# Kernel optimization log

Hardware: AMD Instinct MI355X
Metric: run time of the kernel (lower is better)

## Reference

```python
import jax, jax.numpy as jnp
import numpy as np

EPS = 1e-7


def setup_inputs() -> dict:
    key = jax.random.key(0)
    kx, kw, kv, kp = jax.random.split(key, 4)
    B, H, Wd, d, V, O = 4, 64, 64, 64, 64, 64
    X = jax.random.normal(kx, (B, H, Wd, d), dtype=jnp.float32)
    W = jax.random.normal(kw, (d, V), dtype=jnp.float32)
    # positive variances (kmeans-style init in original); avoid near-zero divisors
    variance = jax.random.uniform(kv, (d, V), dtype=jnp.float32) + 0.5
    weight = jax.random.normal(kp, (d, O), dtype=jnp.float32) * (1.0 / np.sqrt(d))
    return {"X": X, "W": W, "variance": variance, "weight": weight}


def reference(X, W, variance, weight):
    B, H, Wd, d = X.shape
    V = W.shape[1]
    HW = H * Wd
    Xf = X.reshape(B, HW, d)
    # Faithful replication of torch code: extend = tile(X, V) over last axis,
    # then reshape (d*V) -> (d, V) with k = a*V + c, so the X component at
    # grid position (a, c) is X[..., (a*V + c) % d].
    idx = (jnp.arange(d)[:, None] * V + jnp.arange(V)[None, :]) % d  # (d, V)
    Xg = Xf[:, :, idx]                      # (B, HW, d, V)
    q1 = (Xg - W) / variance                # (B, HW, d, V), broadcast (d,V)
    q = jnp.sum(q1 * q1, axis=2)            # (B, HW, V) squared Mahalanobis-ish dist
    q = q - jnp.min(q, axis=-1, keepdims=True)
    Q = jnp.exp(-0.5 * q)
    Q = Q / jnp.sum(Q, axis=-1, keepdims=True)          # soft assignment (B, HW, V)
    # Raw row-major reinterpretation (B, HW, d*V) -> (B, d, HW, V), as in torch
    z = q1.reshape(B, d, HW, V)
    zQ = z * Q[:, None, :, :]                            # (B, d, HW, V)
    z = jnp.sum(zQ, axis=2)                              # (B, d, V)
    Qsum = jnp.sum(Q, axis=1)                            # (B, V)
    z = (z + EPS) / (Qsum[:, None, :] + EPS)
    norm = jnp.sum(z * z, axis=1, keepdims=True)         # (B, 1, V)
    Z = z / norm                                          # (B, d, V)
    Adj = jnp.einsum('bdv,bdu->bvu', Z, Z)               # (B, V, V)
    out = jnp.einsum('bdv,do->bvo', Z, weight)           # (B, V, O)
    out = jnp.einsum('bvu,buo->bvo', Adj, out)           # (B, V, O)
    Zo = jax.nn.relu(out)
    Xn = jnp.einsum('bnv,bvo->bno', Q, Zo)               # (B, HW, O)
    return Xn.reshape(B, H, Wd, -1).transpose(0, 3, 1, 2)  # (B, O, H, W)
```

## Files before the change

### kernel.cpp

```cpp
#include <hip/hip_runtime.h>

#define HW 4096
#define EPSF 1e-7f

#define WS_S1  0
#define WS_S2P 16384
#define WS_QSP 32768
#define WS_Z   49152
#define WS_ZO  65536
#define WS_Q   81920

__device__ __forceinline__ void xr4(float4& v) {
    v.x += __shfl_xor(v.x, 16); v.y += __shfl_xor(v.y, 16);
    v.z += __shfl_xor(v.z, 16); v.w += __shfl_xor(v.w, 16);
    v.x += __shfl_xor(v.x, 32); v.y += __shfl_xor(v.y, 32);
    v.z += __shfl_xor(v.z, 32); v.w += __shfl_xor(v.w, 32);
}

__global__ __launch_bounds__(512) void kA(const float* __restrict__ X,
                                          const float* __restrict__ Wm,
                                          const float* __restrict__ var,
                                          float* __restrict__ ws) {
    int b = blockIdx.x >> 6, l = blockIdx.x & 63;
    int t = threadIdx.x;
    int wv = t >> 6, j = t & 63;
    int lane16 = t & 15, r0 = t >> 4;

    __shared__ __align__(16) float invl[64][64];
    __shared__ __align__(16) float wivl[64][64];
    __shared__ __align__(16) float abcA[64];
    __shared__ __align__(16) float abcB[64];
    __shared__ __align__(16) float abcC[64];
    __shared__ float red[3][8][64];
    __shared__ float4 red4[3][8][16];

    {
        float a = 0.f, bq = 0.f, c = 0.f;
#pragma unroll
        for (int k = 0; k < 8; k++) {
            int i = wv * 8 + k;
            float v   = var[i * 64 + j];
            float wvv = Wm[i * 64 + j];
            float iv  = 1.0f / v;
            invl[i][j] = iv; wivl[i][j] = wvv * iv;
            float iv2 = iv * iv;
            a += iv2; bq += wvv * iv2; c += wvv * wvv * iv2;
        }
        red[0][wv][j] = a; red[1][wv][j] = bq; red[2][wv][j] = c;
    }
    __syncthreads();
    if (t < 64) {
        float t0 = 0.f, t1 = 0.f, t2 = 0.f;
#pragma unroll
        for (int w = 0; w < 8; w++) { t0 += red[0][w][j]; t1 += red[1][w][j]; t2 += red[2][w][j]; }
        abcA[j] = t0; abcB[j] = t1; abcC[j] = t2;
    }
    __syncthreads();

    float4 A4 = *(const float4*)&abcA[lane16 * 4];
    float4 B4 = *(const float4*)&abcB[lane16 * 4];
    float4 C4 = *(const float4*)&abcC[lane16 * 4];
    float4 s1 = {0,0,0,0}, s2 = {0,0,0,0}, qsm = {0,0,0,0};
#pragma unroll
    for (int half = 0; half < 2; half++) {
        int rr = r0 + half * 32;
        int n  = l * 64 + rr;
        float4 x = *(const float4*)&X[((size_t)(b * HW) + n) * 64 + lane16 * 4];
        float4 q;
        q.x = fmaf(fmaf(A4.x, x.x, -2.0f * B4.x), x.x, C4.x);
        q.y = fmaf(fmaf(A4.y, x.y, -2.0f * B4.y), x.y, C4.y);
        q.z = fmaf(fmaf(A4.z, x.z, -2.0f * B4.z), x.z, C4.z);
        q.w = fmaf(fmaf(A4.w, x.w, -2.0f * B4.w), x.w, C4.w);
        float m = fminf(fminf(q.x, q.y), fminf(q.z, q.w));
        m = fminf(m, __shfl_xor(m, 1)); m = fminf(m, __shfl_xor(m, 2));
        m = fminf(m, __shfl_xor(m, 4)); m = fminf(m, __shfl_xor(m, 8));
        float4 e;
        e.x = __expf(-0.5f * (q.x - m)); e.y = __expf(-0.5f * (q.y - m));
        e.z = __expf(-0.5f * (q.z - m)); e.w = __expf(-0.5f * (q.w - m));
        float s = e.x + e.y + e.z + e.w;
        s += __shfl_xor(s, 1); s += __shfl_xor(s, 2);
        s += __shfl_xor(s, 4); s += __shfl_xor(s, 8);
        float rs = 1.0f / s;
        float4 Q4; Q4.x = e.x * rs; Q4.y = e.y * rs; Q4.z = e.z * rs; Q4.w = e.w * rs;
        *(float4*)&ws[WS_Q + ((size_t)(b * HW) + n) * 64 + lane16 * 4] = Q4;
        float4 iv4 = *(const float4*)&invl[rr][lane16 * 4];
        float4 wv4 = *(const float4*)&wivl[rr][lane16 * 4];
        s1.x = fmaf(iv4.x, Q4.x, s1.x); s1.y = fmaf(iv4.y, Q4.y, s1.y);
        s1.z = fmaf(iv4.z, Q4.z, s1.z); s1.w = fmaf(iv4.w, Q4.w, s1.w);
        s2.x = fmaf(wv4.x, Q4.x, s2.x); s2.y = fmaf(wv4.y, Q4.y, s2.y);
        s2.z = fmaf(wv4.z, Q4.z, s2.z); s2.w = fmaf(wv4.w, Q4.w, s2.w);
        qsm.x += Q4.x; qsm.y += Q4.y; qsm.z += Q4.z; qsm.w += Q4.w;
    }
    xr4(s1); xr4(s2); xr4(qsm);
    if ((t & 63) < 16) {
        red4[0][wv][lane16] = s1; red4[1][wv][lane16] = s2; red4[2][wv][lane16] = qsm;
    }
    __syncthreads();
    if (t < 64) {
        int jg = j >> 2, cc = j & 3;
        float t0 = 0.f, t1 = 0.f, t2 = 0.f;
#pragma unroll
        for (int w = 0; w < 8; w++) {
            t0 += ((const float*)&red4[0][w][jg])[cc];
            t1 += ((const float*)&red4[1][w][jg])[cc];
            t2 += ((const float*)&red4[2][w][jg])[cc];
        }
        int idx = (b * 64 + l) * 64 + j;
        ws[WS_S1  + idx] = t0;
        ws[WS_S2P + idx] = t1;
        ws[WS_QSP + idx] = t2;
    }
}

__global__ __launch_bounds__(512) void kB(const float* __restrict__ X,
                                          float* __restrict__ ws) {
    int b = blockIdx.x >> 6, h = blockIdx.x & 63;
    int t = threadIdx.x;
    int wv = t >> 6, j = t & 63;
    int lane16 = t & 15, lg = t >> 4;
    __shared__ float4 red4[3][8][16];
    float4 acc = {0,0,0,0}, ps2 = {0,0,0,0}, pqs = {0,0,0,0};
#pragma unroll
    for (int half = 0; half < 2; half++) {
        int l = lg + half * 32;
        float4 x  = *(const float4*)&X[((size_t)(b * HW) + h * 64 + l) * 64 + lane16 * 4];
        int idx = (b * 64 + l) * 64 + lane16 * 4;
        float4 s1 = *(const float4*)&ws[WS_S1 + idx];
        float4 a2 = *(const float4*)&ws[WS_S2P + idx];
        float4 a3 = *(const float4*)&ws[WS_QSP + idx];
        acc.x = fmaf(x.x, s1.x, acc.x); acc.y = fmaf(x.y, s1.y, acc.y);
        acc.z = fmaf(x.z, s1.z, acc.z); acc.w = fmaf(x.w, s1.w, acc.w);
        ps2.x += a2.x; ps2.y += a2.y; ps2.z += a2.z; ps2.w += a2.w;
        pqs.x += a3.x; pqs.y += a3.y; pqs.z += a3.z; pqs.w += a3.w;
    }
    xr4(acc); xr4(ps2); xr4(pqs);
    if ((t & 63) < 16) {
        red4[0][wv][lane16] = acc; red4[1][wv][lane16] = ps2; red4[2][wv][lane16] = pqs;
    }
    __syncthreads();
    if (t < 64) {
        int jg = j >> 2, cc = j & 3;
        float a = 0.f, s2 = 0.f, q = 0.f;
#pragma unroll
        for (int w = 0; w < 8; w++) {
            a  += ((const float*)&red4[0][w][jg])[cc];
            s2 += ((const float*)&red4[1][w][jg])[cc];
            q  += ((const float*)&red4[2][w][jg])[cc];
        }
        ws[WS_Z + (b * 64 + h) * 64 + j] = (a - s2 + EPSF) / (q + EPSF);
    }
}

__global__ __launch_bounds__(512) void kCD(const float* __restrict__ weight,
                                           float* __restrict__ ws) {
    int b = blockIdx.x >> 6, v = blockIdx.x & 63;
    int w8 = threadIdx.x >> 6, j = threadIdx.x & 63;
    __shared__ float zl[64][65];
    __shared__ float wl[64][65];
    __shared__ float red[8][64];
    __shared__ float sN[64], sin2[64], ghat[64], yv[64];
#pragma unroll
    for (int k = 0; k < 2; k++) {
        int fidx = (k * 512 + threadIdx.x) * 4;
        int r = fidx >> 6, cc = fidx & 63;
        float4 zv = *(const float4*)&ws[WS_Z + b * 4096 + fidx];
        float4 wv = *(const float4*)&weight[fidx];
        zl[r][cc] = zv.x; zl[r][cc+1] = zv.y; zl[r][cc+2] = zv.z; zl[r][cc+3] = zv.w;
        wl[r][cc] = wv.x; wl[r][cc+1] = wv.y; wl[r][cc+2] = wv.z; wl[r][cc+3] = wv.w;
    }
    __syncthreads();
    {
        float na = 0.f;
#pragma unroll
        for (int k = 0; k < 8; k++) { float zz = zl[w8 * 8 + k][j]; na = fmaf(zz, zz, na); }
        red[w8][j] = na;
        __syncthreads();
        if (threadIdx.x < 64) {
            float s = 0.f;
#pragma unroll
            for (int tt = 0; tt < 8; tt++) s += red[tt][j];
            sN[j] = s; sin2[j] = 1.0f / (s * s);
        }
        __syncthreads();
    }
    {
        float g = 0.f;
#pragma unroll
        for (int k = 0; k < 8; k++) { int d = w8 * 8 + k; g = fmaf(zl[d][v], zl[d][j], g); }
        red[w8][j] = g;
        __syncthreads();
        if (threadIdx.x < 64) {
            float s = 0.f;
#pragma unroll
            for (int tt = 0; tt < 8; tt++) s += red[tt][j];
            ghat[j] = s * sin2[j];
        }
        __syncthreads();
    }
    {
        float y = 0.f;
#pragma unroll
        for (int k = 0; k < 8; k++) { int u = w8 * 8 + k; y = fmaf(ghat[u], zl[j][u], y); }
        red[w8][j] = y;
        __syncthreads();
        if (threadIdx.x < 64) {
            float s = 0.f;
#pragma unroll
            for (int tt = 0; tt < 8; tt++) s += red[tt][j];
            yv[j] = s;
        }
        __syncthreads();
    }
    {
        float a = 0.f;
#pragma unroll
        for (int k = 0; k < 8; k++) { int d = w8 * 8 + k; a = fmaf(yv[d], wl[d][j], a); }
        red[w8][j] = a;
        __syncthreads();
        if (threadIdx.x < 64) {
            float s = 0.f;
#pragma unroll
            for (int tt = 0; tt < 8; tt++) s += red[tt][j];
            float r = s / sN[v];
            r = r > 0.f ? r : 0.f;
            ws[WS_ZO + (b * 64 + v) * 64 + j] = r;
        }
    }
}

__global__ __launch_bounds__(512) void kF(const float* __restrict__ ws,
                                          float* __restrict__ out) {
    int b = blockIdx.x >> 6, tb = blockIdx.x & 63;
    int nbase = tb * 64;
    int w8 = threadIdx.x >> 6, lane = threadIdx.x & 63;
    int o8 = w8 * 8;
    __shared__ float qs[64][65];
    __shared__ __align__(16) float zo[64][68];
#pragma unroll
    for (int k = 0; k < 2; k++) {
        int fidx = (k * 512 + threadIdx.x) * 4;
        int r = fidx >> 6, cc = fidx & 63;
        float4 qv = *(const float4*)&ws[WS_Q + ((size_t)(b * HW) + nbase + r) * 64 + cc];
        qs[r][cc] = qv.x; qs[r][cc+1] = qv.y; qs[r][cc+2] = qv.z; qs[r][cc+3] = qv.w;
        float4 zv = *(const float4*)&ws[WS_ZO + b * 4096 + fidx];
        zo[r][cc] = zv.x; zo[r][cc+1] = zv.y; zo[r][cc+2] = zv.z; zo[r][cc+3] = zv.w;
    }
    __syncthreads();
    float acc[8];
#pragma unroll
    for (int k = 0; k < 8; k++) acc[k] = 0.f;
#pragma unroll
    for (int v = 0; v < 64; v++) {
        float qv = qs[lane][v];
        float4 z0 = *(const float4*)&zo[v][o8];
        float4 z1 = *(const float4*)&zo[v][o8 + 4];
        acc[0] = fmaf(qv, z0.x, acc[0]);
        acc[1] = fmaf(qv, z0.y, acc[1]);
        acc[2] = fmaf(qv, z0.z, acc[2]);
        acc[3] = fmaf(qv, z0.w, acc[3]);
        acc[4] = fmaf(qv, z1.x, acc[4]);
        acc[5] = fmaf(qv, z1.y, acc[5]);
        acc[6] = fmaf(qv, z1.z, acc[6]);
        acc[7] = fmaf(qv, z1.w, acc[7]);
    }
#pragma unroll
    for (int k = 0; k < 8; k++) {
        int o = o8 + k;
        out[(size_t)(b * 64 + o) * HW + nbase + lane] = acc[k];
    }
}

extern "C" void kernel_launch(void* const* d_in, const int* in_sizes, int n_in,
                              void* d_out, int out_size, void* d_ws, size_t ws_size,
                              hipStream_t stream) {
    const float* X      = (const float*)d_in[0];
    const float* Wm     = (const float*)d_in[1];
    const float* var    = (const float*)d_in[2];
    const float* weight = (const float*)d_in[3];
    float* ws  = (float*)d_ws;
    float* out = (float*)d_out;

    kA <<<256, 512, 0, stream>>>(X, Wm, var, ws);
    kB <<<256, 512, 0, stream>>>(X, ws);
    kCD<<<256, 512, 0, stream>>>(weight, ws);
    kF <<<256, 512, 0, stream>>>(ws, out);
}
```

Measured before the change: 21.26 us.

## Recompute soft assignments in final kernel instead of storing Q to workspace

Kernel A no longer writes the full Q matrix (B*HW*64 floats) to the workspace. It writes only the A/B/C coefficient vectors, and the final kernel reads X and recomputes the row softmax on the fly. The prologue of kernel A is also restructured to keep the inverse variances in registers and reduce the coefficients with shuffles, removing the large shared-memory tables. This saves about 4 MB of write traffic plus an equal read, in exchange for redoing the exp/softmax arithmetic in kF.

```diff
diff --git a/kernel.cpp b/kernel.cpp
--- a/kernel.cpp
+++ b/kernel.cpp
@@ -8,13 +8,33 @@
 #define WS_QSP 32768
 #define WS_Z   49152
 #define WS_ZO  65536
-#define WS_Q   81920
+#define WS_ABC 81920
 
 __device__ __forceinline__ void xr4(float4& v) {
     v.x += __shfl_xor(v.x, 16); v.y += __shfl_xor(v.y, 16);
     v.z += __shfl_xor(v.z, 16); v.w += __shfl_xor(v.w, 16);
     v.x += __shfl_xor(v.x, 32); v.y += __shfl_xor(v.y, 32);
     v.z += __shfl_xor(v.z, 32); v.w += __shfl_xor(v.w, 32);
+}
+
+__device__ __forceinline__ float4 row_softmax(float4 x, float4 A4, float4 B4, float4 C4) {
+    float4 q;
+    q.x = fmaf(fmaf(A4.x, x.x, -2.0f * B4.x), x.x, C4.x);
+    q.y = fmaf(fmaf(A4.y, x.y, -2.0f * B4.y), x.y, C4.y);
+    q.z = fmaf(fmaf(A4.z, x.z, -2.0f * B4.z), x.z, C4.z);
+    q.w = fmaf(fmaf(A4.w, x.w, -2.0f * B4.w), x.w, C4.w);
+    float m = fminf(fminf(q.x, q.y), fminf(q.z, q.w));
+    m = fminf(m, __shfl_xor(m, 1)); m = fminf(m, __shfl_xor(m, 2));
+    m = fminf(m, __shfl_xor(m, 4)); m = fminf(m, __shfl_xor(m, 8));
+    float4 e;
+    e.x = __expf(-0.5f * (q.x - m)); e.y = __expf(-0.5f * (q.y - m));
+    e.z = __expf(-0.5f * (q.z - m)); e.w = __expf(-0.5f * (q.w - m));
+    float s = e.x + e.y + e.z + e.w;
+    s += __shfl_xor(s, 1); s += __shfl_xor(s, 2);
+    s += __shfl_xor(s, 4); s += __shfl_xor(s, 8);
+    float rs = 1.0f / s;
+    float4 Q4; Q4.x = e.x * rs; Q4.y = e.y * rs; Q4.z = e.z * rs; Q4.w = e.w * rs;
+    return Q4;
 }
 
 __global__ __launch_bounds__(512) void kA(const float* __restrict__ X,
@@ -25,76 +45,82 @@
     int t = threadIdx.x;
     int wv = t >> 6, j = t & 63;
     int lane16 = t & 15, r0 = t >> 4;
-
-    __shared__ __align__(16) float invl[64][64];
-    __shared__ __align__(16) float wivl[64][64];
-    __shared__ __align__(16) float abcA[64];
-    __shared__ __align__(16) float abcB[64];
-    __shared__ __align__(16) float abcC[64];
-    __shared__ float red[3][8][64];
     __shared__ float4 red4[3][8][16];
-
-    {
-        float a = 0.f, bq = 0.f, c = 0.f;
-#pragma unroll
-        for (int k = 0; k < 8; k++) {
-            int i = wv * 8 + k;
-            float v   = var[i * 64 + j];
-            float wvv = Wm[i * 64 + j];
-            float iv  = 1.0f / v;
-            invl[i][j] = iv; wivl[i][j] = wvv * iv;
-            float iv2 = iv * iv;
-            a += iv2; bq += wvv * iv2; c += wvv * wvv * iv2;
-        }
-        red[0][wv][j] = a; red[1][wv][j] = bq; red[2][wv][j] = c;
-    }
-    __syncthreads();
-    if (t < 64) {
-        float t0 = 0.f, t1 = 0.f, t2 = 0.f;
-#pragma unroll
-        for (int w = 0; w < 8; w++) { t0 += red[0][w][j]; t1 += red[1][w][j]; t2 += red[2][w][j]; }
-        abcA[j] = t0; abcB[j] = t1; abcC[j] = t2;
-    }
-    __syncthreads();
-
-    float4 A4 = *(const float4*)&abcA[lane16 * 4];
-    float4 B4 = *(const float4*)&abcB[lane16 * 4];
-    float4 C4 = *(const float4*)&abcC[lane16 * 4];
+    __shared__ float4 abc4[3][16];
+
+    float4 iv0, iv1, wiv0, wiv1;
+    float4 aA = {0,0,0,0}, aB = {0,0,0,0}, aC = {0,0,0,0};
+    {
+        float4 v4 = *(const float4*)&var[r0 * 64 + lane16 * 4];
+        float4 w4 = *(const float4*)&Wm[r0 * 64 + lane16 * 4];
+        iv0.x = 1.0f / v4.x; iv0.y = 1.0f / v4.y; iv0.z = 1.0f / v4.z; iv0.w = 1.0f / v4.w;
+        wiv0.x = w4.x * iv0.x; wiv0.y = w4.y * iv0.y; wiv0.z = w4.z * iv0.z; wiv0.w = w4.w * iv0.w;
+        aA.x = fmaf(iv0.x, iv0.x, aA.x); aA.y = fmaf(iv0.y, iv0.y, aA.y);
+        aA.z = fmaf(iv0.z, iv0.z, aA.z); aA.w = fmaf(iv0.w, iv0.w, aA.w);
+        aB.x = fmaf(wiv0.x, iv0.x, aB.x); aB.y = fmaf(wiv0.y, iv0.y, aB.y);
+        aB.z = fmaf(wiv0.z, iv0.z, aB.z); aB.w = fmaf(wiv0.w, iv0.w, aB.w);
+        aC.x = fmaf(wiv0.x, wiv0.x, aC.x); aC.y = fmaf(wiv0.y, wiv0.y, aC.y);
+        aC.z = fmaf(wiv0.z, wiv0.z, aC.z); aC.w = fmaf(wiv0.w, wiv0.w, aC.w);
+    }
+    {
+        int i = r0 + 32;
+        float4 v4 = *(const float4*)&var[i * 64 + lane16 * 4];
+        float4 w4 = *(const float4*)&Wm[i * 64 + lane16 * 4];
+        iv1.x = 1.0f / v4.x; iv1.y = 1.0f / v4.y; iv1.z = 1.0f / v4.z; iv1.w = 1.0f / v4.w;
+        wiv1.x = w4.x * iv1.x; wiv1.y = w4.y * iv1.y; wiv1.z = w4.z * iv1.z; wiv1.w = w4.w * iv1.w;
+        aA.x = fmaf(iv1.x, iv1.x, aA.x); aA.y = fmaf(iv1.y, iv1.y, aA.y);
+        aA.z = fmaf(iv1.z, iv1.z, aA.z); aA.w = fmaf(iv1.w, iv1.w, aA.w);
+        aB.x = fmaf(wiv1.x, iv1.x, aB.x); aB.y = fmaf(wiv1.y, iv1.y, aB.y);
+        aB.z = fmaf(wiv1.z, iv1.z, aB.z); aB.w = fmaf(wiv1.w, iv1.w, aB.w);
+        aC.x = fmaf(wiv1.x, wiv1.x, aC.x); aC.y = fmaf(wiv1.y, wiv1.y, aC.y);
+        aC.z = fmaf(wiv1.z, wiv1.z, aC.z); aC.w = fmaf(wiv1.w, wiv1.w, aC.w);
+    }
+    xr4(aA); xr4(aB); xr4(aC);
+    if ((t & 63) < 16) { red4[0][wv][lane16] = aA; red4[1][wv][lane16] = aB; red4[2][wv][lane16] = aC; }
+    __syncthreads();
+    if (t < 16) {
+        float4 A = {0,0,0,0}, Bq = {0,0,0,0}, C = {0,0,0,0};
+#pragma unroll
+        for (int w = 0; w < 8; w++) {
+            float4 a = red4[0][w][t], bb = red4[1][w][t], c = red4[2][w][t];
+            A.x += a.x; A.y += a.y; A.z += a.z; A.w += a.w;
+            Bq.x += bb.x; Bq.y += bb.y; Bq.z += bb.z; Bq.w += bb.w;
+            C.x += c.x; C.y += c.y; C.z += c.z; C.w += c.w;
+        }
+        abc4[0][t] = A; abc4[1][t] = Bq; abc4[2][t] = C;
+        if (blockIdx.x == 0) {
+            *(float4*)&ws[WS_ABC + t * 4]       = A;
+            *(float4*)&ws[WS_ABC + 64 + t * 4]  = Bq;
+            *(float4*)&ws[WS_ABC + 128 + t * 4] = C;
+        }
+    }
+    __syncthreads();
+    float4 A4 = abc4[0][lane16], B4 = abc4[1][lane16], C4 = abc4[2][lane16];
+
     float4 s1 = {0,0,0,0}, s2 = {0,0,0,0}, qsm = {0,0,0,0};
-#pragma unroll
-    for (int half = 0; half < 2; half++) {
-        int rr = r0 + half * 32;
-        int n  = l * 64 + rr;
+    {
+        int n = l * 64 + r0;
         float4 x = *(const float4*)&X[((size_t)(b * HW) + n) * 64 + lane16 * 4];
-        float4 q;
-        q.x = fmaf(fmaf(A4.x, x.x, -2.0f * B4.x), x.x, C4.x);
-        q.y = fmaf(fmaf(A4.y, x.y, -2.0f * B4.y), x.y, C4.y);
-        q.z = fmaf(fmaf(A4.z, x.z, -2.0f * B4.z), x.z, C4.z);
-        q.w = fmaf(fmaf(A4.w, x.w, -2.0f * B4.w), x.w, C4.w);
-        float m = fminf(fminf(q.x, q.y), fminf(q.z, q.w));
-        m = fminf(m, __shfl_xor(m, 1)); m = fminf(m, __shfl_xor(m, 2));
-        m = fminf(m, __shfl_xor(m, 4)); m = fminf(m, __shfl_xor(m, 8));
-        float4 e;
-        e.x = __expf(-0.5f * (q.x - m)); e.y = __expf(-0.5f * (q.y - m));
-        e.z = __expf(-0.5f * (q.z - m)); e.w = __expf(-0.5f * (q.w - m));
-        float s = e.x + e.y + e.z + e.w;
-        s += __shfl_xor(s, 1); s += __shfl_xor(s, 2);
-        s += __shfl_xor(s, 4); s += __shfl_xor(s, 8);
-        float rs = 1.0f / s;
-        float4 Q4; Q4.x = e.x * rs; Q4.y = e.y * rs; Q4.z = e.z * rs; Q4.w = e.w * rs;
-        *(float4*)&ws[WS_Q + ((size_t)(b * HW) + n) * 64 + lane16 * 4] = Q4;
-        float4 iv4 = *(const float4*)&invl[rr][lane16 * 4];
-        float4 wv4 = *(const float4*)&wivl[rr][lane16 * 4];
-        s1.x = fmaf(iv4.x, Q4.x, s1.x); s1.y = fmaf(iv4.y, Q4.y, s1.y);
-        s1.z = fmaf(iv4.z, Q4.z, s1.z); s1.w = fmaf(iv4.w, Q4.w, s1.w);
-        s2.x = fmaf(wv4.x, Q4.x, s2.x); s2.y = fmaf(wv4.y, Q4.y, s2.y);
-        s2.z = fmaf(wv4.z, Q4.z, s2.z); s2.w = fmaf(wv4.w, Q4.w, s2.w);
+        float4 Q4 = row_softmax(x, A4, B4, C4);
+        s1.x = fmaf(iv0.x, Q4.x, s1.x); s1.y = fmaf(iv0.y, Q4.y, s1.y);
+        s1.z = fmaf(iv0.z, Q4.z, s1.z); s1.w = fmaf(iv0.w, Q4.w, s1.w);
+        s2.x = fmaf(wiv0.x, Q4.x, s2.x); s2.y = fmaf(wiv0.y, Q4.y, s2.y);
+        s2.z = fmaf(wiv0.z, Q4.z, s2.z); s2.w = fmaf(wiv0.w, Q4.w, s2.w);
         qsm.x += Q4.x; qsm.y += Q4.y; qsm.z += Q4.z; qsm.w += Q4.w;
     }
+    {
+        int n = l * 64 + r0 + 32;
+        float4 x = *(const float4*)&X[((size_t)(b * HW) + n) * 64 + lane16 * 4];
+        float4 Q4 = row_softmax(x, A4, B4, C4);
+        s1.x = fmaf(iv1.x, Q4.x, s1.x); s1.y = fmaf(iv1.y, Q4.y, s1.y);
+        s1.z = fmaf(iv1.z, Q4.z, s1.z); s1.w = fmaf(iv1.w, Q4.w, s1.w);
+        s2.x = fmaf(wiv1.x, Q4.x, s2.x); s2.y = fmaf(wiv1.y, Q4.y, s2.y);
+        s2.z = fmaf(wiv1.z, Q4.z, s2.z); s2.w = fmaf(wiv1.w, Q4.w, s2.w);
+        qsm.x += Q4.x; qsm.y += Q4.y; qsm.z += Q4.z; qsm.w += Q4.w;
+    }
     xr4(s1); xr4(s2); xr4(qsm);
-    if ((t & 63) < 16) {
-        red4[0][wv][lane16] = s1; red4[1][wv][lane16] = s2; red4[2][wv][lane16] = qsm;
-    }
+    __syncthreads();
+    if ((t & 63) < 16) { red4[0][wv][lane16] = s1; red4[1][wv][lane16] = s2; red4[2][wv][lane16] = qsm; }
     __syncthreads();
     if (t < 64) {
         int jg = j >> 2, cc = j & 3;
@@ -228,30 +254,48 @@
     }
 }
 
-__global__ __launch_bounds__(512) void kF(const float* __restrict__ ws,
+__global__ __launch_bounds__(512) void kF(const float* __restrict__ X,
+                                          const float* __restrict__ ws,
                                           float* __restrict__ out) {
     int b = blockIdx.x >> 6, tb = blockIdx.x & 63;
     int nbase = tb * 64;
-    int w8 = threadIdx.x >> 6, lane = threadIdx.x & 63;
+    int t = threadIdx.x;
+    int w8 = t >> 6, j = t & 63;
+    int lane16 = t & 15, r0 = t >> 4;
     int o8 = w8 * 8;
     __shared__ float qs[64][65];
     __shared__ __align__(16) float zo[64][68];
+
+    float4 A4 = *(const float4*)&ws[WS_ABC + lane16 * 4];
+    float4 B4 = *(const float4*)&ws[WS_ABC + 64 + lane16 * 4];
+    float4 C4 = *(const float4*)&ws[WS_ABC + 128 + lane16 * 4];
+
 #pragma unroll
     for (int k = 0; k < 2; k++) {
-        int fidx = (k * 512 + threadIdx.x) * 4;
+        int fidx = (k * 512 + t) * 4;
         int r = fidx >> 6, cc = fidx & 63;
-        float4 qv = *(const float4*)&ws[WS_Q + ((size_t)(b * HW) + nbase + r) * 64 + cc];
-        qs[r][cc] = qv.x; qs[r][cc+1] = qv.y; qs[r][cc+2] = qv.z; qs[r][cc+3] = qv.w;
         float4 zv = *(const float4*)&ws[WS_ZO + b * 4096 + fidx];
         zo[r][cc] = zv.x; zo[r][cc+1] = zv.y; zo[r][cc+2] = zv.z; zo[r][cc+3] = zv.w;
     }
-    __syncthreads();
+#pragma unroll
+    for (int half = 0; half < 2; half++) {
+        int rr = r0 + half * 32;
+        int n = nbase + rr;
+        float4 x = *(const float4*)&X[((size_t)(b * HW) + n) * 64 + lane16 * 4];
+        float4 Q4 = row_softmax(x, A4, B4, C4);
+        qs[rr][lane16 * 4]     = Q4.x;
+        qs[rr][lane16 * 4 + 1] = Q4.y;
+        qs[rr][lane16 * 4 + 2] = Q4.z;
+        qs[rr][lane16 * 4 + 3] = Q4.w;
+    }
+    __syncthreads();
+
     float acc[8];
 #pragma unroll
     for (int k = 0; k < 8; k++) acc[k] = 0.f;
 #pragma unroll
     for (int v = 0; v < 64; v++) {
-        float qv = qs[lane][v];
+        float qv = qs[j][v];
         float4 z0 = *(const float4*)&zo[v][o8];
         float4 z1 = *(const float4*)&zo[v][o8 + 4];
         acc[0] = fmaf(qv, z0.x, acc[0]);
@@ -266,7 +310,7 @@
 #pragma unroll
     for (int k = 0; k < 8; k++) {
         int o = o8 + k;
-        out[(size_t)(b * 64 + o) * HW + nbase + lane] = acc[k];
+        out[(size_t)(b * 64 + o) * HW + nbase + j] = acc[k];
     }
 }
 
@@ -283,5 +327,5 @@
     kA <<<256, 512, 0, stream>>>(X, Wm, var, ws);
     kB <<<256, 512, 0, stream>>>(X, ws);
     kCD<<<256, 512, 0, stream>>>(weight, ws);
-    kF <<<256, 512, 0, stream>>>(ws, out);
-}
+    kF <<<256, 512, 0, stream>>>(X, ws, out);
+}
```

After: 21.69 us. +2.0%, slower.
